# Kernel optimization log

Hardware: AMD Instinct MI355X
Metric: run time of the kernel (lower is better)

Reference implementation:

```python
import jax, jax.numpy as jnp
from jax import lax
import numpy as np

S, B, T, N, FJ, H, MF, M = 8, 64, 64, 16, 32, 128, 16, 8
NN = S + M  # total machine-graph nodes
EPS = 1e-5
SLOPE = 0.2


def layernorm(x, g, b):
    mu = x.mean(-1, keepdims=True)
    var = ((x - mu) ** 2).mean(-1, keepdims=True)
    return (x - mu) / jnp.sqrt(var + EPS) * g + b


def gat(adj, x, W, a):
    # dense GAT layer: x [..., N, Fin], adj [..., N, N]
    h = x @ W  # [..., N, O]
    O = W.shape[1]
    f1 = h @ a[:O]  # [..., N]
    f2 = h @ a[O:]
    e = jax.nn.leaky_relu(f1[..., :, None] + f2[..., None, :], SLOPE)
    e = jnp.where(adj > 0, e, jnp.float32(-1e9))
    return jax.nn.softmax(e, axis=-1) @ h


def job_enc(adj, x, Ws, As):
    t = jnp.tanh(gat(adj, x, Ws[0], As[0]))
    t = jnp.tanh(gat(adj, t, Ws[1], As[1]) + t)
    t = jnp.tanh(gat(adj, t, Ws[2], As[2]) + t)
    t = jnp.tanh(t + gat(adj, t, Ws[3], As[3]))
    return t.mean(-2)  # mean over ops dim


def lstm_last(x, Wih, Whh, b):
    # x: [Bx, T, H]; returns final hidden state [Bx, H]
    xs = jnp.einsum('bti,gi->tbg', x, Wih) + b  # [T, Bx, 4H]
    h0 = jnp.zeros((x.shape[0], Whh.shape[1]), x.dtype)

    def step(carry, xt):
        h, c = carry
        g = xt + h @ Whh.T
        i, f, gg, o = jnp.split(g, 4, axis=-1)
        c = jax.nn.sigmoid(f) * c + jax.nn.sigmoid(i) * jnp.tanh(gg)
        h = jax.nn.sigmoid(o) * jnp.tanh(c)
        return (h, c), None

    (h, _), _ = lax.scan(step, (h0, h0), xs)
    return h


def setup_inputs() -> dict:
    key = jax.random.key(0)
    ks = jax.random.split(key, 32)

    def adj(k, shape):
        a = jax.random.bernoulli(k, 0.4, shape).astype(jnp.int32)
        return jnp.maximum(a, jnp.eye(shape[-1], dtype=jnp.int32))

    mfeat = jax.random.normal(ks[4], (B, NN, MF), jnp.float32)
    # stage nodes (first S) have feature[...,0] > 0; machine nodes < 0
    mfeat = mfeat.at[:, :S, 0].set(jnp.abs(mfeat[:, :S, 0]) + 0.1)
    mfeat = mfeat.at[:, S:, 0].set(-jnp.abs(mfeat[:, S:, 0]) - 0.1)

    sc = 0.08
    inp = {
        'j_stages_f': jax.random.normal(ks[0], (S, B, T, N, FJ), jnp.float32),
        'j_stages_a': adj(ks[1], (S, B, T, N, N)),
        'j_machine_f': jax.random.normal(ks[2], (B, M, N, FJ), jnp.float32),
        'j_machine_a': adj(ks[3], (B, M, N, N)),
        'machine_f': mfeat,
        'machine_a': adj(ks[5], (B, NN, NN)),
        'jg1_W': jax.random.normal(ks[6], (FJ, H), jnp.float32) * sc,
        'jgW': jax.random.normal(ks[7], (3, H, H), jnp.float32) * sc,
        'jga': jax.random.normal(ks[8], (4, 2 * H), jnp.float32) * sc,
        'lstm_Wih': jax.random.normal(ks[9], (4 * H, H), jnp.float32) * sc,
        'lstm_Whh': jax.random.normal(ks[10], (4 * H, H), jnp.float32) * sc,
        'lstm_b': jnp.zeros((4 * H,), jnp.float32),
        'mfe_W': jax.random.normal(ks[11], (MF, H), jnp.float32) * sc,
        'mfe_b': jnp.zeros((H,), jnp.float32),
        'n2_g': jnp.ones((H,), jnp.float32),
        'n2_b': jnp.zeros((H,), jnp.float32),
        'me_W': jax.random.normal(ks[12], (2 * H, H), jnp.float32) * sc,
        'me_b': jnp.zeros((H,), jnp.float32),
        'n3_g': jnp.ones((H,), jnp.float32),
        'n3_b': jnp.zeros((H,), jnp.float32),
        'mgW': jax.random.normal(ks[13], (4, H, H), jnp.float32) * sc,
        'mga': jax.random.normal(ks[14], (4, 2 * H), jnp.float32) * sc,
        'mng': jnp.ones((4, H), jnp.float32),
        'mnb': jnp.zeros((4, H), jnp.float32),
    }
    return inp


def reference(j_stages_f, j_stages_a, j_machine_f, j_machine_a, machine_f,
              machine_a, jg1_W, jgW, jga, lstm_Wih, lstm_Whh, lstm_b,
              mfe_W, mfe_b, n2_g, n2_b, me_W, me_b, n3_g, n3_b,
              mgW, mga, mng, mnb):
    Ws = [jg1_W, jgW[0], jgW[1], jgW[2]]
    As = [jga[0], jga[1], jga[2], jga[3]]

    # per-stage job encoding + LSTM over job sequence
    stage_emb = jax.vmap(lambda a, f: job_enc(a, f, Ws, As))(j_stages_a, j_stages_f)  # [S,B,T,H]
    hlast = lstm_last(stage_emb.reshape(S * B, T, H), lstm_Wih, lstm_Whh, lstm_b)
    j_encoded = hlast.reshape(S, B, H).transpose(1, 0, 2)  # [B,S,H]

    # machine-side job graph encoding (shared encoder)
    jm = job_enc(j_machine_a, j_machine_f, Ws, As)  # [B,M,H]

    # machine node embedding
    mfh = jnp.tanh(layernorm(machine_f @ mfe_W + mfe_b, n2_g, n2_b))  # [B,NN,H]

    # static routing: first S nodes -> stage contexts, rest -> machine contexts
    ctx = jnp.concatenate([j_encoded, jm], axis=1)  # [B,NN,H]
    nodes = jnp.concatenate([mfh, ctx], axis=-1)  # [B,NN,2H]
    nodes = jnp.tanh(layernorm(nodes @ me_W + me_b, n3_g, n3_b))

    h = nodes
    prev = None
    for k in range(4):
        h2 = layernorm(gat(machine_a, h, mgW[k], mga[k]), mng[k], mnb[k])
        if k != 0:
            h2 = h2 + prev
        h = jnp.tanh(h2)
        prev = h
    return h.mean(axis=1)  # [B, H]
```

## Files before the change

kernel.cpp:

```cpp
#include <hip/hip_runtime.h>
#include <hip/hip_bf16.h>
#include <math.h>

#define S_ 8
#define B_ 64
#define T_ 64
#define N_ 16
#define FJ_ 32
#define H_ 128
#define MF_ 16
#define M_ 8
#define SB_ 512
#define G1_ 32768
#define G2_ 512

#define CPAD 132
#define PPAD 17

typedef short bf16x8 __attribute__((ext_vector_type(8)));
typedef short bf16x4 __attribute__((ext_vector_type(4)));
typedef float f32x4 __attribute__((ext_vector_type(4)));
typedef unsigned short u16;

__device__ __forceinline__ u16 f2bf(float f) {
  union { float f; unsigned u; } v; v.f = f;
  unsigned r = v.u + 0x7FFFu + ((v.u >> 16) & 1u);
  return (u16)(r >> 16);
}
__device__ __forceinline__ unsigned pk2(float lo, float hi) {
  __hip_bfloat162 h2 = __float22bfloat162_rn(make_float2(lo, hi));
  union { __hip_bfloat162 h; unsigned u; } x; x.h = h2; return x.u;
}
__device__ __forceinline__ bf16x4 mkfrag(unsigned a, unsigned b) {
  union { bf16x4 v; unsigned u[2]; } x; x.u[0] = a; x.u[1] = b; return x.v;
}
__device__ __forceinline__ f32x4 mfma16(bf16x4 a, bf16x4 b, f32x4 c) {
#if __has_builtin(__builtin_amdgcn_mfma_f32_16x16x16bf16_1k)
  return __builtin_amdgcn_mfma_f32_16x16x16bf16_1k(a, b, c, 0, 0, 0);
#else
  asm("v_mfma_f32_16x16x16_bf16 %0, %1, %2, %0" : "+v"(c) : "v"(a), "v"(b));
  return c;
#endif
}
__device__ __forceinline__ float frcp(float x) {
#if __has_builtin(__builtin_amdgcn_rcpf)
  return __builtin_amdgcn_rcpf(x);
#else
  return 1.f / x;
#endif
}
__device__ __forceinline__ float frsq(float x) {
#if __has_builtin(__builtin_amdgcn_rsqf)
  return __builtin_amdgcn_rsqf(x);
#else
  return rsqrtf(x);
#endif
}
__device__ __forceinline__ float ftanh(float x) {
  float e = __expf(2.f * x);
  return fmaf(-2.f, frcp(e + 1.f), 1.f);
}
__device__ __forceinline__ float sigmoidf_(float x) {
  return frcp(1.f + __expf(-x));
}

__device__ __forceinline__ void fma8(float (&acc)[8], float xv, float4 wa, float4 wb) {
  acc[0] = fmaf(xv, wa.x, acc[0]); acc[1] = fmaf(xv, wa.y, acc[1]);
  acc[2] = fmaf(xv, wa.z, acc[2]); acc[3] = fmaf(xv, wa.w, acc[3]);
  acc[4] = fmaf(xv, wb.x, acc[4]); acc[5] = fmaf(xv, wb.y, acc[5]);
  acc[6] = fmaf(xv, wb.z, acc[6]); acc[7] = fmaf(xv, wb.w, acc[7]);
}
__device__ __forceinline__ float grp16_sum(float v) {
#pragma unroll
  for (int m = 1; m < 16; m <<= 1) v += __shfl_xor(v, m);
  return v;
}
__device__ __forceinline__ float grp16_max(float v) {
#pragma unroll
  for (int m = 1; m < 16; m <<= 1) v = fmaxf(v, __shfl_xor(v, m));
  return v;
}
__device__ __forceinline__ void ln_row(float (&v)[8], const float* gw, const float* bw, int j0) {
  float s1 = 0.f, s2 = 0.f;
#pragma unroll
  for (int c = 0; c < 8; ++c) { s1 += v[c]; s2 += v[c] * v[c]; }
  s1 = grp16_sum(s1); s2 = grp16_sum(s2);
  float mu = s1 * (1.f / 128.f);
  float var = s2 * (1.f / 128.f) - mu * mu;
  float rstd = frsq(var + 1e-5f);
#pragma unroll
  for (int c = 0; c < 8; ++c) v[c] = (v[c] - mu) * rstd * gw[j0 + c] + bw[j0 + c];
}

__global__ __launch_bounds__(256) void pack_w_kernel(
    const float* __restrict__ W0, const float* __restrict__ W123,
    const float* __restrict__ jga,
    const float* __restrict__ Wih, const float* __restrict__ Whh,
    u16* __restrict__ wpk0, u16* __restrict__ wpkL,
    u16* __restrict__ wpkIH, u16* __restrict__ wpkHH)
{
  int idx = blockIdx.x * 256 + threadIdx.x;
  if (idx < 4608) {
    int e = idx & 3, l = (idx >> 2) & 63, t = idx >> 8;
    int n = t >> 1, kk = t & 1;
    int q = l >> 4, cc = l & 15;
    int k = 16 * kk + 4 * q + e;
    float v = 0.f;
    if (n < 8) v = W0[k * 128 + 16 * n + cc];
    else if (cc < 2) {
      const float* a = jga + cc * 128;
      float s = 0.f;
      for (int j = 0; j < 128; ++j) s += W0[k * 128 + j] * a[j];
      v = s;
    }
    wpk0[idx] = f2bf(v);
  } else if (idx < 59904) {
    int id = idx - 4608;
    int e = id & 3, l = (id >> 2) & 63;
    int t2 = id >> 8;
    int t = t2 % 72, layer = t2 / 72;
    int n = t >> 3, kk = t & 7;
    int q = l >> 4, cc = l & 15;
    int k = 16 * kk + 4 * q + e;
    const float* W = W123 + (size_t)layer * 16384;
    float v = 0.f;
    if (n < 8) v = W[k * 128 + 16 * n + cc];
    else if (cc < 2) {
      const float* a = jga + (layer + 1) * 256 + cc * 128;
      float s = 0.f;
      for (int j = 0; j < 128; ++j) s += W[k * 128 + j] * a[j];
      v = s;
    }
    wpkL[id] = f2bf(v);
  } else if (idx < 125440) {
    int id = idx - 59904;
    int e = id & 7, l = (id >> 3) & 63, kk = (id >> 9) & 3, n = id >> 11;
    int gate = 16 * n + (l & 15), k = 32 * kk + 8 * (l >> 4) + e;
    wpkIH[id] = f2bf(Wih[gate * 128 + k]);
  } else if (idx < 190976) {
    int id = idx - 125440;
    int e = id & 7, l = (id >> 3) & 63, kk = (id >> 9) & 3, n = id >> 11;
    int gate = 16 * n + (l & 15), k = 32 * kk + 8 * (l >> 4) + e;
    wpkHH[id] = f2bf(Whh[gate * 128 + k]);
  }
}

__global__ __launch_bounds__(512) __attribute__((amdgpu_waves_per_eu(4, 8)))
void gat_mfma_kernel(
    const float* __restrict__ xinA, const int* __restrict__ adjA,
    float* __restrict__ outmA, u16* __restrict__ outbfA,
    const float* __restrict__ xinB, const int* __restrict__ adjB,
    float* __restrict__ outmB, u16* __restrict__ outbfB,
    const u16* __restrict__ wpk0, const u16* __restrict__ wpkL)
{
  __shared__ __align__(16) u16 wbuf[18432];
  __shared__ __align__(16) float fbuf[8][32];

  const int wv = threadIdx.x >> 6;
  const int l = threadIdx.x & 63;
  const int c = l & 15, q = l >> 4;
  float* fb = fbuf[wv];

  const float* xin; const int* adjin; float* outm; u16* outbf; int g;
  if (blockIdx.x < G1_ / 8) {
    xin = xinA; adjin = adjA; outm = outmA; outbf = outbfA;
    g = blockIdx.x * 8 + wv;
  } else {
    xin = xinB; adjin = adjB; outm = outmB; outbf = outbfB;
    g = (blockIdx.x - G1_ / 8) * 8 + wv;
  }

  auto stage = [&](const u16* src, int nbytes) {
    const float4* s4 = (const float4*)src;
    float4* d4 = (float4*)wbuf;
    int n16 = nbytes >> 4;
    for (int i = threadIdx.x; i < n16; i += 512) d4[i] = s4[i];
  };

  int4 A1 = *(const int4*)(adjin + (size_t)g * 256 + c * 16 + 4 * q);

  f32x4 res[8];
  bf16x4 hfrag[8];

  auto softmax_pv = [&](f32x4 Cf, bool resid) {
    if (c < 2) *(f32x4*)(fb + c * 16 + 4 * q) = Cf;
    float f1v = fb[c];
    float4 f2v = *(const float4*)(fb + 16 + 4 * q);
    float ev[4] = {f1v + f2v.x, f1v + f2v.y, f1v + f2v.z, f1v + f2v.w};
#pragma unroll
    for (int e = 0; e < 4; ++e) ev[e] = (ev[e] >= 0.f) ? ev[e] : 0.2f * ev[e];
    ev[0] = (A1.x > 0) ? ev[0] : -1e9f;
    ev[1] = (A1.y > 0) ? ev[1] : -1e9f;
    ev[2] = (A1.z > 0) ? ev[2] : -1e9f;
    ev[3] = (A1.w > 0) ? ev[3] : -1e9f;
    float mx = fmaxf(fmaxf(ev[0], ev[1]), fmaxf(ev[2], ev[3]));
    mx = fmaxf(mx, __shfl_xor(mx, 16));
    mx = fmaxf(mx, __shfl_xor(mx, 32));
    float sm = 0.f;
#pragma unroll
    for (int e = 0; e < 4; ++e) { ev[e] = __expf(ev[e] - mx); sm += ev[e]; }
    sm += __shfl_xor(sm, 16);
    sm += __shfl_xor(sm, 32);
    float zinv = frcp(sm);
    bf16x4 pfrag = mkfrag(pk2(ev[0] * zinv, ev[1] * zinv), pk2(ev[2] * zinv, ev[3] * zinv));
#pragma unroll
    for (int m = 0; m < 8; ++m) {
      f32x4 o = resid ? res[m] : (f32x4){0.f, 0.f, 0.f, 0.f};
      o = mfma16(hfrag[m], pfrag, o);
      f32x4 t;
      t[0] = ftanh(o[0]); t[1] = ftanh(o[1]); t[2] = ftanh(o[2]); t[3] = ftanh(o[3]);
      res[m] = t;
    }
  };

  stage(wpk0, 9216);
  __syncthreads();
  {
    bf16x4 xf[2];
    const float* xg = xin + (size_t)g * 512 + c * 32 + 4 * q;
    float4 x1 = *(const float4*)xg;
    float4 x2 = *(const float4*)(xg + 16);
    xf[0] = mkfrag(pk2(x1.x, x1.y), pk2(x1.z, x1.w));
    xf[1] = mkfrag(pk2(x2.x, x2.y), pk2(x2.z, x2.w));
#pragma unroll
    for (int n = 0; n < 8; ++n) {
      f32x4 Ch = (f32x4){0.f, 0.f, 0.f, 0.f};
#pragma unroll
      for (int kk = 0; kk < 2; ++kk) {
        bf16x4 wf = *(const bf16x4*)(wbuf + ((n * 2 + kk) * 64 + l) * 4);
        Ch = mfma16(xf[kk], wf, Ch);
      }
      hfrag[n] = mkfrag(pk2(Ch[0], Ch[1]), pk2(Ch[2], Ch[3]));
    }
    f32x4 Cf = (f32x4){0.f, 0.f, 0.f, 0.f};
#pragma unroll
    for (int kk = 0; kk < 2; ++kk) {
      bf16x4 wf = *(const bf16x4*)(wbuf + ((16 + kk) * 64 + l) * 4);
      Cf = mfma16(xf[kk], wf, Cf);
    }
    softmax_pv(Cf, false);
  }
  __syncthreads();

#pragma unroll 1
  for (int layer = 1; layer < 4; ++layer) {
    stage(wpkL + (size_t)(layer - 1) * 18432, 36864);
    __syncthreads();
    bf16x4 xf[8];
#pragma unroll
    for (int kk = 0; kk < 8; ++kk)
      xf[kk] = mkfrag(pk2(res[kk][0], res[kk][1]), pk2(res[kk][2], res[kk][3]));
#pragma unroll
    for (int n = 0; n < 8; ++n) {
      f32x4 Ch = (f32x4){0.f, 0.f, 0.f, 0.f};
#pragma unroll
      for (int kk = 0; kk < 8; ++kk) {
        bf16x4 wf = *(const bf16x4*)(wbuf + ((n * 8 + kk) * 64 + l) * 4);
        Ch = mfma16(xf[kk], wf, Ch);
      }
      hfrag[n] = mkfrag(pk2(Ch[0], Ch[1]), pk2(Ch[2], Ch[3]));
    }
    f32x4 Cf = (f32x4){0.f, 0.f, 0.f, 0.f};
#pragma unroll
    for (int kk = 0; kk < 8; ++kk) {
      bf16x4 wf = *(const bf16x4*)(wbuf + ((64 + kk) * 64 + l) * 4);
      Cf = mfma16(xf[kk], wf, Cf);
    }
    softmax_pv(Cf, true);
    __syncthreads();
  }

  u16* tb = wbuf + wv * 2176;
#pragma unroll
  for (int m = 0; m < 8; ++m) {
    uint2 u;
    u.x = pk2(res[m][0], res[m][1]);
    u.y = pk2(res[m][2], res[m][3]);
    *(uint2*)(tb + c * 136 + 16 * m + 4 * q) = u;
  }
  {
    float s0 = 0.f, s1 = 0.f;
#pragma unroll
    for (int node = 0; node < 16; ++node) {
      unsigned u = *(const unsigned*)(tb + node * 136 + 2 * l);
      union { unsigned u; float f; } lo, hi;
      lo.u = u << 16; hi.u = u & 0xffff0000u;
      s0 += lo.f; s1 += hi.f;
    }
    s0 *= 0.0625f; s1 *= 0.0625f;
    if (outm) *(float2*)(outm + (size_t)g * 128 + 2 * l) = make_float2(s0, s1);
    *(unsigned*)(outbf + (size_t)g * 128 + 2 * l) = pk2(s0, s1);
  }
}

__global__ __launch_bounds__(512) __attribute__((amdgpu_waves_per_eu(1, 2)))
void lstm_fused_kernel(
    const u16* __restrict__ emb_bf,
    const u16* __restrict__ wpkIH, const u16* __restrict__ wpkHH,
    const float* __restrict__ bvec,
    float* __restrict__ hlast)
{
  __shared__ unsigned hbuf[2][1024];
  const int tid = threadIdx.x;
  const int w = tid >> 6, l = tid & 63;
  const int c = l & 15, q = l >> 4;
  const int ce = c & 7;
  const int seq0 = blockIdx.x * 8;
  const int swz = (c & 7) << 2;

  bf16x8 aih[4][4], ahh[4][4];
#pragma unroll
  for (int m = 0; m < 4; ++m)
#pragma unroll
    for (int kk = 0; kk < 4; ++kk) {
      int n = 8 * m + w;
      aih[m][kk] = *(const bf16x8*)(wpkIH + ((size_t)((n * 4 + kk) * 64 + l)) * 8);
      ahh[m][kk] = *(const bf16x8*)(wpkHH + ((size_t)((n * 4 + kk) * 64 + l)) * 8);
    }
  float bias[4][4];
#pragma unroll
  for (int m = 0; m < 4; ++m)
#pragma unroll
    for (int r = 0; r < 4; ++r) bias[m][r] = bvec[128 * m + 16 * w + 4 * q + r];

  hbuf[0][tid] = 0u;
  hbuf[0][512 + tid] = 0u;
  __syncthreads();

  const u16* xbase = emb_bf + ((size_t)(seq0 + ce)) * 64 * 128 + q * 8;

  bf16x8 xnxt[4];
  f32x4 accih[4];
  {
    bf16x8 xf[4];
#pragma unroll
    for (int kk = 0; kk < 4; ++kk) xf[kk] = *(const bf16x8*)(xbase + kk * 32);
#pragma unroll
    for (int m = 0; m < 4; ++m) {
      f32x4 a = (f32x4){0.f, 0.f, 0.f, 0.f};
#pragma unroll
      for (int kk = 0; kk < 4; ++kk)
        a = __builtin_amdgcn_mfma_f32_16x16x32_bf16(aih[m][kk], xf[kk], a, 0, 0, 0);
      accih[m] = a;
    }
#pragma unroll
    for (int kk = 0; kk < 4; ++kk) xnxt[kk] = *(const bf16x8*)(xbase + 128 + kk * 32);
  }

  float cst[4] = {0.f, 0.f, 0.f, 0.f};
  float hv[4] = {0.f, 0.f, 0.f, 0.f};
  int pb = 0;
#pragma unroll 1
  for (int t = 0; t < T_; ++t) {
    bf16x8 hf[4];
#pragma unroll
    for (int kk = 0; kk < 4; ++kk) {
      int j0 = (16 * kk + 4 * q) ^ swz;
      hf[kk] = *(const bf16x8*)&hbuf[pb][c * 64 + j0];
    }
    f32x4 acc[4];
#pragma unroll
    for (int m = 0; m < 4; ++m) {
      f32x4 a = accih[m];
#pragma unroll
      for (int kk = 0; kk < 4; ++kk)
        a = __builtin_amdgcn_mfma_f32_16x16x32_bf16(ahh[m][kk], hf[kk], a, 0, 0, 0);
      acc[m] = a;
    }
#pragma unroll
    for (int r = 0; r < 4; ++r) {
      float ig = acc[0][r] + bias[0][r];
      float fg = acc[1][r] + bias[1][r];
      float gg = acc[2][r] + bias[2][r];
      float og = acc[3][r] + bias[3][r];
      cst[r] = sigmoidf_(fg) * cst[r] + sigmoidf_(ig) * ftanh(gg);
      hv[r] = sigmoidf_(og) * ftanh(cst[r]);
    }
    {
      int j0 = (8 * w + 2 * q) ^ swz;
      uint2 u2; u2.x = pk2(hv[0], hv[1]); u2.y = pk2(hv[2], hv[3]);
      *(uint2*)&hbuf[pb ^ 1][c * 64 + j0] = u2;
    }
    if (t < T_ - 1) {
#pragma unroll
      for (int m = 0; m < 4; ++m) {
        f32x4 a = (f32x4){0.f, 0.f, 0.f, 0.f};
#pragma unroll
        for (int kk = 0; kk < 4; ++kk)
          a = __builtin_amdgcn_mfma_f32_16x16x32_bf16(aih[m][kk], xnxt[kk], a, 0, 0, 0);
        accih[m] = a;
      }
      if (t < T_ - 2) {
        const u16* xr = xbase + (size_t)(t + 2) * 128;
#pragma unroll
        for (int kk = 0; kk < 4; ++kk) xnxt[kk] = *(const bf16x8*)(xr + kk * 32);
      }
    }
    __syncthreads();
    pb ^= 1;
  }
  if (c < 8) {
#pragma unroll
    for (int r = 0; r < 4; ++r)
      hlast[((size_t)(seq0 + ce)) * 128 + 16 * w + 4 * q + r] = hv[r];
  }
}

__global__ __launch_bounds__(256) __attribute__((amdgpu_waves_per_eu(2, 4)))
void machine_kernel(
    const float* __restrict__ machine_f, const int* __restrict__ machine_a,
    const float* __restrict__ hlast, const float* __restrict__ jm,
    const float* __restrict__ mfe_W, const float* __restrict__ mfe_b,
    const float* __restrict__ n2_g, const float* __restrict__ n2_b,
    const float* __restrict__ me_W, const float* __restrict__ me_b,
    const float* __restrict__ n3_g, const float* __restrict__ n3_b,
    const float* __restrict__ mgW, const float* __restrict__ mga,
    const float* __restrict__ mng, const float* __restrict__ mnb,
    float* __restrict__ outp)
{
  __shared__ float mf[256];
  __shared__ int adjs[256];
  __shared__ __align__(16) float ctx[16 * CPAD];
  __shared__ __align__(16) float mfh[16 * CPAD];
  __shared__ __align__(16) float cur[16 * CPAD];
  __shared__ __align__(16) float tmp[16 * CPAD];
  __shared__ __align__(16) float prevb[16 * CPAD];
  __shared__ float pm[16 * PPAD];
  __shared__ float f1s[16], f2s[16];

  const int b = blockIdx.x;
  const int tid = threadIdx.x;
  const int i = tid >> 4;
  const int jb = tid & 15;
  const int j0 = jb << 3;

  mf[tid] = machine_f[(size_t)b * 256 + tid];
  adjs[tid] = machine_a[(size_t)b * 256 + tid];
  {
    const float* src = (i < 8) ? (hlast + ((size_t)i * B_ + b) * H_)
                               : (jm + ((size_t)b * M_ + (i - 8)) * H_);
    *(float4*)(ctx + i * CPAD + j0) = ((const float4*)src)[jb * 2];
    *(float4*)(ctx + i * CPAD + j0 + 4) = ((const float4*)src)[jb * 2 + 1];
  }
  __syncthreads();

  {
    float acc[8];
#pragma unroll
    for (int c = 0; c < 8; ++c) acc[c] = 0.f;
#pragma unroll
    for (int k = 0; k < MF_; ++k) {
      float xv = mf[i * 16 + k];
      float4 wa = *(const float4*)(mfe_W + (size_t)k * H_ + j0);
      float4 wb = *(const float4*)(mfe_W + (size_t)k * H_ + j0 + 4);
      fma8(acc, xv, wa, wb);
    }
#pragma unroll
    for (int c = 0; c < 8; ++c) acc[c] += mfe_b[j0 + c];
    ln_row(acc, n2_g, n2_b, j0);
#pragma unroll
    for (int c = 0; c < 8; ++c) mfh[i * CPAD + j0 + c] = ftanh(acc[c]);
  }
  __syncthreads();

  {
    float acc[8];
#pragma unroll
    for (int c = 0; c < 8; ++c) acc[c] = 0.f;
#pragma unroll 4
    for (int k = 0; k < H_; ++k) {
      float xv = mfh[i * CPAD + k];
      float4 wa = *(const float4*)(me_W + (size_t)k * H_ + j0);
      float4 wb = *(const float4*)(me_W + (size_t)k * H_ + j0 + 4);
      fma8(acc, xv, wa, wb);
    }
#pragma unroll 4
    for (int k = 0; k < H_; ++k) {
      float xv = ctx[i * CPAD + k];
      float4 wa = *(const float4*)(me_W + (size_t)(128 + k) * H_ + j0);
      float4 wb = *(const float4*)(me_W + (size_t)(128 + k) * H_ + j0 + 4);
      fma8(acc, xv, wa, wb);
    }
#pragma unroll
    for (int c = 0; c < 8; ++c) acc[c] += me_b[j0 + c];
    ln_row(acc, n3_g, n3_b, j0);
#pragma unroll
    for (int c = 0; c < 8; ++c) cur[i * CPAD + j0 + c] = ftanh(acc[c]);
  }
  __syncthreads();

  for (int ll = 0; ll < 4; ++ll) {
    const float* W = mgW + (size_t)ll * H_ * H_;
    const float* a0 = mga + ll * 256;
    const float* a1 = a0 + 128;

    float acc[8];
#pragma unroll
    for (int c = 0; c < 8; ++c) acc[c] = 0.f;
#pragma unroll 4
    for (int k = 0; k < H_; ++k) {
      float xv = cur[i * CPAD + k];
      float4 wa = *(const float4*)(W + (size_t)k * H_ + j0);
      float4 wb = *(const float4*)(W + (size_t)k * H_ + j0 + 4);
      fma8(acc, xv, wa, wb);
    }
    *(float4*)(tmp + i * CPAD + j0) = make_float4(acc[0], acc[1], acc[2], acc[3]);
    *(float4*)(tmp + i * CPAD + j0 + 4) = make_float4(acc[4], acc[5], acc[6], acc[7]);

    float p1 = 0.f, p2 = 0.f;
#pragma unroll
    for (int c = 0; c < 8; ++c) {
      p1 = fmaf(acc[c], a0[j0 + c], p1);
      p2 = fmaf(acc[c], a1[j0 + c], p2);
    }
    p1 = grp16_sum(p1); p2 = grp16_sum(p2);
    if (jb == 0) { f1s[i] = p1; f2s[i] = p2; }
    __syncthreads();

    {
      int jc = jb;
      float e = f1s[i] + f2s[jc];
      e = (e >= 0.f) ? e : 0.2f * e;
      if (adjs[i * 16 + jc] <= 0) e = -1e9f;
      float mxv = grp16_max(e);
      float ex = __expf(e - mxv);
      float smv = grp16_sum(ex);
      pm[i * PPAD + jc] = ex * frcp(smv);
    }
    __syncthreads();

    float o[8];
#pragma unroll
    for (int c = 0; c < 8; ++c) o[c] = 0.f;
#pragma unroll
    for (int k = 0; k < 16; ++k) {
      float pv = pm[i * PPAD + k];
      float4 ha = *(const float4*)(tmp + k * CPAD + j0);
      float4 hb = *(const float4*)(tmp + k * CPAD + j0 + 4);
      fma8(o, pv, ha, hb);
    }
    ln_row(o, mng + ll * H_, mnb + ll * H_, j0);
#pragma unroll
    for (int c = 0; c < 8; ++c) {
      float v = o[c] + ((ll > 0) ? prevb[i * CPAD + j0 + c] : 0.f);
      v = ftanh(v);
      cur[i * CPAD + j0 + c] = v;
      prevb[i * CPAD + j0 + c] = v;
    }
    __syncthreads();
  }

  if (tid < 128) {
    float s = 0.f;
#pragma unroll
    for (int r = 0; r < 16; ++r) s += cur[r * CPAD + tid];
    outp[(size_t)b * H_ + tid] = s * (1.f / 16.f);
  }
}

extern "C" void kernel_launch(void* const* d_in, const int* in_sizes, int n_in,
                              void* d_out, int out_size, void* d_ws, size_t ws_size,
                              hipStream_t stream) {
  const float* j_stages_f  = (const float*)d_in[0];
  const int*   j_stages_a  = (const int*)d_in[1];
  const float* j_machine_f = (const float*)d_in[2];
  const int*   j_machine_a = (const int*)d_in[3];
  const float* machine_f   = (const float*)d_in[4];
  const int*   machine_a   = (const int*)d_in[5];
  const float* jg1_W       = (const float*)d_in[6];
  const float* jgW         = (const float*)d_in[7];
  const float* jga         = (const float*)d_in[8];
  const float* lstm_Wih    = (const float*)d_in[9];
  const float* lstm_Whh    = (const float*)d_in[10];
  const float* lstm_b      = (const float*)d_in[11];
  const float* mfe_W       = (const float*)d_in[12];
  const float* mfe_b       = (const float*)d_in[13];
  const float* n2_g        = (const float*)d_in[14];
  const float* n2_b        = (const float*)d_in[15];
  const float* me_W        = (const float*)d_in[16];
  const float* me_b        = (const float*)d_in[17];
  const float* n3_g        = (const float*)d_in[18];
  const float* n3_b        = (const float*)d_in[19];
  const float* mgW         = (const float*)d_in[20];
  const float* mga         = (const float*)d_in[21];
  const float* mng         = (const float*)d_in[22];
  const float* mnb         = (const float*)d_in[23];
  float* out = (float*)d_out;

  char* ws = (char*)d_ws;
  u16*   emb_bf  = (u16*)ws;
  u16*   jmbf    = (u16*)(ws + 8388608);
  float* jm      = (float*)(ws + 8519680);
  float* hlast   = (float*)(ws + 8781824);
  u16*   wpk0    = (u16*)(ws + 9043968);
  u16*   wpkL    = (u16*)(ws + 9053184);
  u16*   wpkIH   = (u16*)(ws + 9163776);
  u16*   wpkHH   = (u16*)(ws + 9294848);

  pack_w_kernel<<<746, 256, 0, stream>>>(jg1_W, jgW, jga, lstm_Wih, lstm_Whh,
                                         wpk0, wpkL, wpkIH, wpkHH);
  gat_mfma_kernel<<<G1_ / 8 + G2_ / 8, 512, 0, stream>>>(
      j_stages_f, j_stages_a, (float*)nullptr, emb_bf,
      j_machine_f, j_machine_a, jm, jmbf, wpk0, wpkL);
  lstm_fused_kernel<<<SB_ / 8, 512, 0, stream>>>(emb_bf, wpkIH, wpkHH, lstm_b, hlast);
  machine_kernel<<<B_, 256, 0, stream>>>(machine_f, machine_a, hlast, jm,
                                         mfe_W, mfe_b, n2_g, n2_b, me_W, me_b,
                                         n3_g, n3_b, mgW, mga, mng, mnb, out);
}
```

Baseline: 325.8 us.

## Double-buffer GAT layer weights in LDS with async global-to-LDS loads

Replaces the synchronous register-staged copy of each layer's weights into shared memory with direct global_load_lds transfers split into two halves. The next layer's weight halves are prefetched while the current layer's MFMA and softmax work runs, using vmcnt waits and barriers to sequence them. Waves-per-EU hints are also lowered. This aims to hide the weight-staging latency, at the cost of fragile manual waitcnt ordering. It also relies on the adjacency load being counted in vmcnt.

```diff
diff --git a/kernel.cpp b/kernel.cpp
--- a/kernel.cpp
+++ b/kernel.cpp
@@ -21,6 +21,16 @@
 typedef short bf16x4 __attribute__((ext_vector_type(4)));
 typedef float f32x4 __attribute__((ext_vector_type(4)));
 typedef unsigned short u16;
+
+#define WAITVM0 { asm volatile("s_waitcnt vmcnt(0)" ::: "memory"); __builtin_amdgcn_sched_barrier(0); }
+#define WAITVM2 { asm volatile("s_waitcnt vmcnt(2)" ::: "memory"); __builtin_amdgcn_sched_barrier(0); }
+#define BARRIER { __builtin_amdgcn_s_barrier(); __builtin_amdgcn_sched_barrier(0); }
+
+__device__ __forceinline__ void gload16(const u16* g, u16* l) {
+  __builtin_amdgcn_global_load_lds(
+      (const __attribute__((address_space(1))) unsigned int*)g,
+      (__attribute__((address_space(3))) unsigned int*)l, 16, 0, 0);
+}
 
 __device__ __forceinline__ u16 f2bf(float f) {
   union { float f; unsigned u; } v; v.f = f;
@@ -145,7 +155,7 @@
   }
 }
 
-__global__ __launch_bounds__(512) __attribute__((amdgpu_waves_per_eu(4, 8)))
+__global__ __launch_bounds__(512) __attribute__((amdgpu_waves_per_eu(2, 4)))
 void gat_mfma_kernel(
     const float* __restrict__ xinA, const int* __restrict__ adjA,
     float* __restrict__ outmA, u16* __restrict__ outbfA,
@@ -156,10 +166,13 @@
   __shared__ __align__(16) u16 wbuf[18432];
   __shared__ __align__(16) float fbuf[8][32];
 
-  const int wv = threadIdx.x >> 6;
-  const int l = threadIdx.x & 63;
+  const int tid = threadIdx.x;
+  const int wv = tid >> 6;
+  const int l = tid & 63;
   const int c = l & 15, q = l >> 4;
   float* fb = fbuf[wv];
+  u16* Abuf = wbuf;
+  u16* Bbuf = wbuf + 8192;
 
   const float* xin; const int* adjin; float* outm; u16* outbf; int g;
   if (blockIdx.x < G1_ / 8) {
@@ -170,11 +183,20 @@
     g = (blockIdx.x - G1_ / 8) * 8 + wv;
   }
 
-  auto stage = [&](const u16* src, int nbytes) {
-    const float4* s4 = (const float4*)src;
-    float4* d4 = (float4*)wbuf;
-    int n16 = nbytes >> 4;
-    for (int i = threadIdx.x; i < n16; i += 512) d4[i] = s4[i];
+  auto issueL0 = [&]() {
+    gload16(wpk0 + (size_t)tid * 8, Abuf + tid * 8);
+    if (tid < 64) gload16(wpk0 + (size_t)(512 + tid) * 8, Abuf + (512 + tid) * 8);
+  };
+  auto issueH1 = [&](int L) {
+    const u16* s = wpkL + (size_t)(L - 1) * 18432;
+    gload16(s + (size_t)tid * 8, Abuf + tid * 8);
+    gload16(s + (size_t)(512 + tid) * 8, Abuf + (512 + tid) * 8);
+  };
+  auto issueH2 = [&](int L) {
+    const u16* s = wpkL + (size_t)(L - 1) * 18432 + 8192;
+    gload16(s + (size_t)tid * 8, Bbuf + tid * 8);
+    gload16(s + (size_t)(512 + tid) * 8, Bbuf + (512 + tid) * 8);
+    if (tid < 256) gload16(s + (size_t)(1024 + tid) * 8, Bbuf + (1024 + tid) * 8);
   };
 
   int4 A1 = *(const int4*)(adjin + (size_t)g * 256 + c * 16 + 4 * q);
@@ -213,8 +235,9 @@
     }
   };
 
-  stage(wpk0, 9216);
-  __syncthreads();
+  issueL0();
+  WAITVM0; BARRIER;
+  issueH2(1);
   {
     bf16x4 xf[2];
     const float* xg = xin + (size_t)g * 512 + c * 32 + 4 * q;
@@ -227,7 +250,7 @@
       f32x4 Ch = (f32x4){0.f, 0.f, 0.f, 0.f};
 #pragma unroll
       for (int kk = 0; kk < 2; ++kk) {
-        bf16x4 wf = *(const bf16x4*)(wbuf + ((n * 2 + kk) * 64 + l) * 4);
+        bf16x4 wf = *(const bf16x4*)(Abuf + ((n * 2 + kk) * 64 + l) * 4);
         Ch = mfma16(xf[kk], wf, Ch);
       }
       hfrag[n] = mkfrag(pk2(Ch[0], Ch[1]), pk2(Ch[2], Ch[3]));
@@ -235,27 +258,27 @@
     f32x4 Cf = (f32x4){0.f, 0.f, 0.f, 0.f};
 #pragma unroll
     for (int kk = 0; kk < 2; ++kk) {
-      bf16x4 wf = *(const bf16x4*)(wbuf + ((16 + kk) * 64 + l) * 4);
+      bf16x4 wf = *(const bf16x4*)(Abuf + ((16 + kk) * 64 + l) * 4);
       Cf = mfma16(xf[kk], wf, Cf);
     }
     softmax_pv(Cf, false);
   }
-  __syncthreads();
+  BARRIER;
+  issueH1(1);
 
 #pragma unroll 1
   for (int layer = 1; layer < 4; ++layer) {
-    stage(wpkL + (size_t)(layer - 1) * 18432, 36864);
-    __syncthreads();
+    WAITVM2; BARRIER;
     bf16x4 xf[8];
 #pragma unroll
     for (int kk = 0; kk < 8; ++kk)
       xf[kk] = mkfrag(pk2(res[kk][0], res[kk][1]), pk2(res[kk][2], res[kk][3]));
 #pragma unroll
-    for (int n = 0; n < 8; ++n) {
+    for (int n = 4; n < 8; ++n) {
       f32x4 Ch = (f32x4){0.f, 0.f, 0.f, 0.f};
 #pragma unroll
       for (int kk = 0; kk < 8; ++kk) {
-        bf16x4 wf = *(const bf16x4*)(wbuf + ((n * 8 + kk) * 64 + l) * 4);
+        bf16x4 wf = *(const bf16x4*)(Bbuf + (((n - 4) * 8 + kk) * 64 + l) * 4);
         Ch = mfma16(xf[kk], wf, Ch);
       }
       hfrag[n] = mkfrag(pk2(Ch[0], Ch[1]), pk2(Ch[2], Ch[3]));
@@ -263,11 +286,24 @@
     f32x4 Cf = (f32x4){0.f, 0.f, 0.f, 0.f};
 #pragma unroll
     for (int kk = 0; kk < 8; ++kk) {
-      bf16x4 wf = *(const bf16x4*)(wbuf + ((64 + kk) * 64 + l) * 4);
+      bf16x4 wf = *(const bf16x4*)(Bbuf + ((32 + kk) * 64 + l) * 4);
       Cf = mfma16(xf[kk], wf, Cf);
     }
+    WAITVM0; BARRIER;
+    if (layer < 3) issueH2(layer + 1);
+#pragma unroll
+    for (int n = 0; n < 4; ++n) {
+      f32x4 Ch = (f32x4){0.f, 0.f, 0.f, 0.f};
+#pragma unroll
+      for (int kk = 0; kk < 8; ++kk) {
+        bf16x4 wf = *(const bf16x4*)(Abuf + ((n * 8 + kk) * 64 + l) * 4);
+        Ch = mfma16(xf[kk], wf, Ch);
+      }
+      hfrag[n] = mkfrag(pk2(Ch[0], Ch[1]), pk2(Ch[2], Ch[3]));
+    }
     softmax_pv(Cf, true);
-    __syncthreads();
+    BARRIER;
+    if (layer < 3) issueH1(layer + 1);
   }
 
   u16* tb = wbuf + wv * 2176;
```

Result: no change. 323.3 us (-0.8%).
